# Kernel optimization log

Hardware: AMD Instinct MI355X
Metric: run time of the kernel (lower is better)

Reference implementation:

```python
import jax, jax.numpy as jnp
import numpy as np

N_HEAD = 16
LN_EPS = 1e-5


def _layernorm(x, g, b):
    mu = jnp.mean(x, axis=-1, keepdims=True)
    var = jnp.mean(jnp.square(x - mu), axis=-1, keepdims=True)
    return (x - mu) * jax.lax.rsqrt(var + LN_EPS) * g + b


def setup_inputs() -> dict:
    key = jax.random.key(0)
    ks = jax.random.split(key, 12)
    B, S, D = 2, 2048, 1024
    F = 4 * D
    std = 0.02
    return {
        "x": jax.random.normal(ks[0], (B, S, D), jnp.float32),
        "w_attn": jax.random.normal(ks[1], (D, 3 * D), jnp.float32) * std,
        "b_attn": jnp.zeros((3 * D,), jnp.float32),
        "w_o": jax.random.normal(ks[2], (D, D), jnp.float32) * std,
        "b_o": jnp.zeros((D,), jnp.float32),
        "ln1_g": jnp.ones((D,), jnp.float32),
        "ln1_b": jnp.zeros((D,), jnp.float32),
        "w_fc": jax.random.normal(ks[3], (D, F), jnp.float32) * std,
        "b_fc": jnp.zeros((F,), jnp.float32),
        "w_pr": jax.random.normal(ks[4], (F, D), jnp.float32) * std,
        "b_pr": jnp.zeros((D,), jnp.float32),
        "ln2_g": jnp.ones((D,), jnp.float32),
        "ln2_b": jnp.zeros((D,), jnp.float32),
    }


def reference(x, w_attn, b_attn, w_o, b_o, ln1_g, ln1_b,
              w_fc, b_fc, w_pr, b_pr, ln2_g, ln2_b):
    B, S, D = x.shape
    H = N_HEAD
    hd = D // H

    # --- attention ---
    qkv = x @ w_attn + b_attn                      # [B,S,3D]
    q, k, v = jnp.split(qkv, 3, axis=-1)
    q = q.reshape(B, S, H, hd).transpose(0, 2, 1, 3)  # [B,H,S,hd]
    k = k.reshape(B, S, H, hd).transpose(0, 2, 1, 3)
    v = v.reshape(B, S, H, hd).transpose(0, 2, 1, 3)

    # scores in fp32, scaled by sqrt(head_dim) (scale=True)
    w = jnp.einsum('bhqd,bhkd->bhqk', q.astype(jnp.float32),
                   k.astype(jnp.float32)) / jnp.sqrt(jnp.float32(hd))
    bias = jnp.tril(jnp.ones((S, S), jnp.float32))     # causal mask slice of registered buffer
    w = w * bias + (-10000.0) * (1.0 - bias)
    a = jax.nn.softmax(w, axis=-1).astype(v.dtype)
    o = jnp.einsum('bhqk,bhkd->bhqd', a, v)            # [B,H,S,hd]
    o = o.transpose(0, 2, 1, 3).reshape(B, S, D)
    a_out = o @ w_o + b_o

    # --- post-LN residual + MLP (gelu, d_ff = 4D) ---
    n = _layernorm(x + a_out, ln1_g, ln1_b)
    m = jax.nn.gelu(n @ w_fc + b_fc, approximate=False) @ w_pr + b_pr
    h = _layernorm(n + m, ln2_g, ln2_b)
    return h
```

## Files before the change

kernel.cpp:

```cpp
#include <hip/hip_runtime.h>
#include <stdint.h>
#include <math.h>


typedef __attribute__((ext_vector_type(4))) float f32x4;
typedef __attribute__((ext_vector_type(8))) short s16x8;

__device__ __forceinline__ float bf2f(short s){
  unsigned u = ((unsigned)(unsigned short)s) << 16;
  return __builtin_bit_cast(float, u);
}
__device__ __forceinline__ short f2bf(float f){
  unsigned u = __builtin_bit_cast(unsigned, f);
  unsigned r = (u + 0x7fffu + ((u >> 16) & 1u)) >> 16;
  return (short)(unsigned short)r;
}

__device__ __forceinline__ void gload_lds16(const void* gp, void* lp){
  __builtin_amdgcn_global_load_lds(
      (__attribute__((address_space(1))) void*)const_cast<void*>(gp),
      (__attribute__((address_space(3))) void*)lp,
      16, 0, 0);
}

__global__ void cvt_f32_bf16(const float* __restrict__ in, short* __restrict__ out, int n){
  int i = (blockIdx.x * blockDim.x + threadIdx.x) * 4;
  if (i < n){
    float4 v = *(const float4*)(in + i);
    short4 o;
    o.x = f2bf(v.x); o.y = f2bf(v.y); o.z = f2bf(v.z); o.w = f2bf(v.w);
    *(short4*)(out + i) = o;
  }
}

__global__ __launch_bounds__(256) void wtrans(const float* __restrict__ in,
                                              short* __restrict__ out, int R, int C){
  __shared__ float tile[32][33];
  int c0 = blockIdx.x * 32, r0 = blockIdx.y * 32;
  int tx = threadIdx.x, ty = threadIdx.y;
  #pragma unroll
  for (int j = 0; j < 4; ++j)
    tile[ty + j*8][tx] = in[(size_t)(r0 + ty + j*8) * C + c0 + tx];
  __syncthreads();
  #pragma unroll
  for (int j = 0; j < 4; ++j)
    out[(size_t)(c0 + ty + j*8) * R + r0 + tx] = f2bf(tile[tx][ty + j*8]);
}

__global__ __launch_bounds__(256) void vtrans(const short* __restrict__ qkv,
                                              short* __restrict__ vt){
  __shared__ short tile[32][33];
  int bh = blockIdx.z; int b = bh >> 4, h = bh & 15;
  int s0 = blockIdx.x * 32, d0 = blockIdx.y * 32;
  int tx = threadIdx.x, ty = threadIdx.y;
  #pragma unroll
  for (int j = 0; j < 4; ++j)
    tile[ty + j*8][tx] = qkv[(size_t)(b*2048 + s0 + ty + j*8) * 3072 + 2048 + h*64 + d0 + tx];
  __syncthreads();
  #pragma unroll
  for (int j = 0; j < 4; ++j)
    vt[(size_t)(bh*64 + d0 + ty + j*8) * 2048 + s0 + tx] = tile[tx][ty + j*8];
}

#define GBM 128
#define GBN 128
#define GBK 64

__global__ __launch_bounds__(256, 4) void gemm_bf16(
    const short* __restrict__ A, const short* __restrict__ BT,
    const float* __restrict__ bias,
    void* __restrict__ out, void* __restrict__ out2,
    void* __restrict__ out3, void* __restrict__ out4,
    int M, int N, int K, int EPI, int KS)
{
  __shared__ short sA[GBM * GBK];
  __shared__ short sB[GBN * GBK];
  const int t = threadIdx.x;
  const int lane = t & 63;
  const int w = t >> 6;
  const int wr = w >> 1, wc = w & 1;
  const int lrow = lane & 15;
  const int lk = lane >> 4;

  const int gx = gridDim.x;
  const int nwg = gx * gridDim.y;
  const int P = blockIdx.y * gx + blockIdx.x;
  const int wg = (P & 7) * (nwg >> 3) + (P >> 3);
  const int m0 = (wg / gx) * GBM, n0 = (wg % gx) * GBN;

  const int Kspl = K / KS;
  const int kbeg = blockIdx.z * Kspl;

  f32x4 acc[4][4] = {};

  for (int kk = kbeg; kk < kbeg + Kspl; kk += GBK){
    __syncthreads();
    #pragma unroll
    for (int r = 0; r < 4; ++r){
      int o = r * 4096 + t * 16;
      int row = o >> 7;
      int phys = (o >> 4) & 7;
      int lsl = phys ^ (row & 7);
      gload_lds16(A + (size_t)(m0 + row) * K + kk + lsl * 8, (char*)sA + o);
    }
    #pragma unroll
    for (int r = 0; r < 4; ++r){
      int o = r * 4096 + t * 16;
      int row = o >> 7;
      int phys = (o >> 4) & 7;
      int lsl = phys ^ (row & 7);
      gload_lds16(BT + (size_t)(n0 + row) * K + kk + lsl * 8, (char*)sB + o);
    }
    __syncthreads();

    #pragma unroll
    for (int kc = 0; kc < 2; ++kc){
      s16x8 af[4], bf[4];
      #pragma unroll
      for (int rt = 0; rt < 4; ++rt){
        int row = wr*64 + rt*16 + lrow;
        int slot = (kc*4 + lk) ^ (row & 7);
        af[rt] = *(const s16x8*)&sA[row*64 + slot*8];
      }
      #pragma unroll
      for (int ct = 0; ct < 4; ++ct){
        int row = wc*64 + ct*16 + lrow;
        int slot = (kc*4 + lk) ^ (row & 7);
        bf[ct] = *(const s16x8*)&sB[row*64 + slot*8];
      }
      #pragma unroll
      for (int rt = 0; rt < 4; ++rt)
        #pragma unroll
        for (int ct = 0; ct < 4; ++ct)
          acc[rt][ct] = __builtin_amdgcn_mfma_f32_16x16x32_bf16(af[rt], bf[ct], acc[rt][ct], 0, 0, 0);
    }
  }

  void* pz = (blockIdx.z == 0) ? out : (blockIdx.z == 1) ? out2
           : (blockIdx.z == 2) ? out3 : out4;
  #pragma unroll
  for (int rt = 0; rt < 4; ++rt){
    #pragma unroll
    for (int ct = 0; ct < 4; ++ct){
      #pragma unroll
      for (int r = 0; r < 4; ++r){
        int row = m0 + wr*64 + rt*16 + lk*4 + r;
        int col = n0 + wc*64 + ct*16 + lrow;
        size_t idx = (size_t)row * N + col;
        if (EPI == 4){
          ((short*)pz)[idx] = f2bf(acc[rt][ct][r]);
        } else {
          float v = acc[rt][ct][r] + bias[col];
          if (EPI == 0){
            ((short*)out)[idx] = f2bf(v);
          } else {
            float g = 0.5f * v * (1.0f + erff(v * 0.70710678118654752f));
            ((short*)out)[idx] = f2bf(g);
          }
        }
      }
    }
  }
}

__global__ __launch_bounds__(256, 2) void attn_kernel(
    const short* __restrict__ qkv, const short* __restrict__ vt,
    short* __restrict__ ob)
{
  const int P = blockIdx.x;
  const int xcd = P & 7;
  const int idx = P >> 3;
  const int raw = idx & 15;
  const int grp = idx >> 4;
  const int pairi = (grp & 2) ? (15 - raw) : raw;
  const int bh = xcd + (grp << 3);
  const int b = bh >> 4, h = bh & 15;
  const int t  = threadIdx.x;
  const int lane = t & 63;
  const int w = t >> 6;
  const int lrow = lane & 15, lk = lane >> 4;

  __shared__ short sK[2][64*64];
  __shared__ short sV[2][64*64];
  __shared__ short sP[4][16][68];

  const size_t kgbase = (size_t)(b*2048)*3072 + 1024 + h*64;
  const size_t vgbase = (size_t)((b*16 + h)*64)*2048;

  s16x8 bones;
  #pragma unroll
  for (int i = 0; i < 8; ++i) bones[i] = (short)0x3F80;

  auto stage = [&](int buf, int k0){
    #pragma unroll
    for (int r2 = 0; r2 < 2; ++r2){
      int o = r2*4096 + t*16;
      int row = o >> 7;
      int lsl = ((o >> 4) & 7) ^ (row & 7);
      gload_lds16(qkv + kgbase + (size_t)(k0 + row)*3072 + lsl*8, (char*)sK[buf] + o);
      gload_lds16(vt  + vgbase + (size_t)row*2048 + k0   + lsl*8, (char*)sV[buf] + o);
    }
  };

  const int qtA = pairi;
  const int qtB = 31 - pairi;
  const int qbaseA = qtA*64 + w*16;
  const int qbaseB = qtB*64 + w*16;

  s16x8 aqA[2], aqB[2];
  #pragma unroll
  for (int kc = 0; kc < 2; ++kc){
    aqA[kc] = *(const s16x8*)(qkv + (size_t)(b*2048 + qbaseA + lrow)*3072 + h*64 + kc*32 + lk*8);
    aqB[kc] = *(const s16x8*)(qkv + (size_t)(b*2048 + qbaseB + lrow)*3072 + h*64 + kc*32 + lk*8);
  }

  f32x4 oaccA[4] = {}, oaccB[4] = {};
  f32x4 sumA = {}, sumB = {};

  const int ntA = qtA + 1;
  const int ntB = qtB + 1;
  stage(0, 0);
  int cur = 0;

  for (int ktile = 0; ktile < ntB; ++ktile){
    const int k0 = ktile * 64;
    if (ktile + 1 < ntB){
      stage(cur ^ 1, k0 + 64);
      asm volatile("s_waitcnt vmcnt(4)" ::: "memory");
    } else {
      asm volatile("s_waitcnt vmcnt(0)" ::: "memory");
    }
    __builtin_amdgcn_s_barrier();
    __builtin_amdgcn_sched_barrier(0);

    {
      f32x4 sacc[4] = {};
      __builtin_amdgcn_s_setprio(1);
      #pragma unroll
      for (int kc = 0; kc < 2; ++kc){
        #pragma unroll
        for (int ct = 0; ct < 4; ++ct){
          int row = ct*16 + lrow;
          int slot = (kc*4 + lk) ^ (row & 7);
          s16x8 bk = *(const s16x8*)&sK[cur][row*64 + slot*8];
          sacc[ct] = __builtin_amdgcn_mfma_f32_16x16x32_bf16(aqB[kc], bk, sacc[ct], 0, 0, 0);
        }
      }
      __builtin_amdgcn_s_setprio(0);

      const bool need_mask = (k0 + 63 > qbaseB);
      #pragma unroll
      for (int ct = 0; ct < 4; ++ct){
        #pragma unroll
        for (int r = 0; r < 4; ++r){
          float v = sacc[ct][r] * 0.125f;
          if (need_mask){
            int qi = qbaseB + lk*4 + r;
            int ki = k0 + ct*16 + lrow;
            if (ki > qi) v = -10000.0f;
          }
          sP[w][lk*4 + r][ct*16 + lrow] = f2bf(__expf(v));
        }
      }

      s16x8 pa[2];
      #pragma unroll
      for (int kc = 0; kc < 2; ++kc)
        pa[kc] = *(const s16x8*)&sP[w][lrow][kc*32 + lk*8];
      __builtin_amdgcn_s_setprio(1);
      #pragma unroll
      for (int dt = 0; dt < 4; ++dt){
        #pragma unroll
        for (int kc = 0; kc < 2; ++kc){
          int row = dt*16 + lrow;
          int slot = (kc*4 + lk) ^ (row & 7);
          s16x8 bv = *(const s16x8*)&sV[cur][row*64 + slot*8];
          oaccB[dt] = __builtin_amdgcn_mfma_f32_16x16x32_bf16(pa[kc], bv, oaccB[dt], 0, 0, 0);
        }
      }
      #pragma unroll
      for (int kc = 0; kc < 2; ++kc)
        sumB = __builtin_amdgcn_mfma_f32_16x16x32_bf16(pa[kc], bones, sumB, 0, 0, 0);
      __builtin_amdgcn_s_setprio(0);
    }

    if (ktile < ntA){
      f32x4 sacc[4] = {};
      __builtin_amdgcn_s_setprio(1);
      #pragma unroll
      for (int kc = 0; kc < 2; ++kc){
        #pragma unroll
        for (int ct = 0; ct < 4; ++ct){
          int row = ct*16 + lrow;
          int slot = (kc*4 + lk) ^ (row & 7);
          s16x8 bk = *(const s16x8*)&sK[cur][row*64 + slot*8];
          sacc[ct] = __builtin_amdgcn_mfma_f32_16x16x32_bf16(aqA[kc], bk, sacc[ct], 0, 0, 0);
        }
      }
      __builtin_amdgcn_s_setprio(0);

      const bool need_mask = (k0 + 63 > qbaseA);
      #pragma unroll
      for (int ct = 0; ct < 4; ++ct){
        #pragma unroll
        for (int r = 0; r < 4; ++r){
          float v = sacc[ct][r] * 0.125f;
          if (need_mask){
            int qi = qbaseA + lk*4 + r;
            int ki = k0 + ct*16 + lrow;
            if (ki > qi) v = -10000.0f;
          }
          sP[w][lk*4 + r][ct*16 + lrow] = f2bf(__expf(v));
        }
      }

      s16x8 pa[2];
      #pragma unroll
      for (int kc = 0; kc < 2; ++kc)
        pa[kc] = *(const s16x8*)&sP[w][lrow][kc*32 + lk*8];
      __builtin_amdgcn_s_setprio(1);
      #pragma unroll
      for (int dt = 0; dt < 4; ++dt){
        #pragma unroll
        for (int kc = 0; kc < 2; ++kc){
          int row = dt*16 + lrow;
          int slot = (kc*4 + lk) ^ (row & 7);
          s16x8 bv = *(const s16x8*)&sV[cur][row*64 + slot*8];
          oaccA[dt] = __builtin_amdgcn_mfma_f32_16x16x32_bf16(pa[kc], bv, oaccA[dt], 0, 0, 0);
        }
      }
      #pragma unroll
      for (int kc = 0; kc < 2; ++kc)
        sumA = __builtin_amdgcn_mfma_f32_16x16x32_bf16(pa[kc], bones, sumA, 0, 0, 0);
      __builtin_amdgcn_s_setprio(0);
    }

    __builtin_amdgcn_sched_barrier(0);
    __builtin_amdgcn_s_barrier();
    cur ^= 1;
  }

  #pragma unroll
  for (int r = 0; r < 4; ++r){
    float invA = 1.0f / sumA[r];
    float invB = 1.0f / sumB[r];
    int rowA = b*2048 + qbaseA + lk*4 + r;
    int rowB = b*2048 + qbaseB + lk*4 + r;
    #pragma unroll
    for (int dt = 0; dt < 4; ++dt){
      int col = h*64 + dt*16 + lrow;
      ob[(size_t)rowA * 1024 + col] = f2bf(oaccA[dt][r] * invA);
      ob[(size_t)rowB * 1024 + col] = f2bf(oaccB[dt][r] * invB);
    }
  }
}

__global__ __launch_bounds__(256) void ln_fused(
    const short* __restrict__ p0, const short* __restrict__ p1,
    const short* __restrict__ p2, const short* __restrict__ p3,
    const float* __restrict__ bias,
    const short* __restrict__ resid_bf, const float* __restrict__ resid_f,
    const float* __restrict__ g, const float* __restrict__ b,
    void* __restrict__ out, int bf16_out)
{
  const int row = blockIdx.x;
  const int t = threadIdx.x;
  const size_t base = (size_t)row*1024 + t*4;
  short4 a0 = *(const short4*)(p0 + base);
  short4 a1 = *(const short4*)(p1 + base);
  short4 a2 = *(const short4*)(p2 + base);
  short4 a3 = *(const short4*)(p3 + base);
  float4 bi = *(const float4*)(bias + t*4);
  float r0, r1, r2, r3;
  if (resid_bf){
    short4 rr = *(const short4*)(resid_bf + base);
    r0 = bf2f(rr.x); r1 = bf2f(rr.y); r2 = bf2f(rr.z); r3 = bf2f(rr.w);
  } else {
    float4 rr = *(const float4*)(resid_f + base);
    r0 = rr.x; r1 = rr.y; r2 = rr.z; r3 = rr.w;
  }
  float v0 = bf2f(a0.x) + bf2f(a1.x) + bf2f(a2.x) + bf2f(a3.x) + bi.x + r0;
  float v1 = bf2f(a0.y) + bf2f(a1.y) + bf2f(a2.y) + bf2f(a3.y) + bi.y + r1;
  float v2 = bf2f(a0.z) + bf2f(a1.z) + bf2f(a2.z) + bf2f(a3.z) + bi.z + r2;
  float v3 = bf2f(a0.w) + bf2f(a1.w) + bf2f(a2.w) + bf2f(a3.w) + bi.w + r3;
  float s = v0 + v1 + v2 + v3;
  float q = v0*v0 + v1*v1 + v2*v2 + v3*v3;
  #pragma unroll
  for (int off = 1; off < 64; off <<= 1){
    s += __shfl_xor(s, off, 64);
    q += __shfl_xor(q, off, 64);
  }
  __shared__ float ss[4], sq[4];
  if ((t & 63) == 0){ ss[t >> 6] = s; sq[t >> 6] = q; }
  __syncthreads();
  s = ss[0] + ss[1] + ss[2] + ss[3];
  q = sq[0] + sq[1] + sq[2] + sq[3];
  float mu = s * (1.0f/1024.0f);
  float var = q * (1.0f/1024.0f) - mu*mu;
  float rs = rsqrtf(var + 1e-5f);
  float4 gg = *(const float4*)(g + t*4);
  float4 bb = *(const float4*)(b + t*4);
  float o0 = (v0 - mu)*rs*gg.x + bb.x;
  float o1 = (v1 - mu)*rs*gg.y + bb.y;
  float o2 = (v2 - mu)*rs*gg.z + bb.z;
  float o3 = (v3 - mu)*rs*gg.w + bb.w;
  if (bf16_out){
    short4 o; o.x = f2bf(o0); o.y = f2bf(o1); o.z = f2bf(o2); o.w = f2bf(o3);
    *(short4*)((short*)out + base) = o;
  } else {
    float4 o = {o0, o1, o2, o3};
    *(float4*)((float*)out + base) = o;
  }
}

extern "C" void kernel_launch(void* const* d_in, const int* in_sizes, int n_in,
                              void* d_out, int out_size, void* d_ws, size_t ws_size,
                              hipStream_t stream) {
  const float* x      = (const float*)d_in[0];
  const float* w_attn = (const float*)d_in[1];
  const float* b_attn = (const float*)d_in[2];
  const float* w_o    = (const float*)d_in[3];
  const float* b_o    = (const float*)d_in[4];
  const float* ln1_g  = (const float*)d_in[5];
  const float* ln1_b  = (const float*)d_in[6];
  const float* w_fc   = (const float*)d_in[7];
  const float* b_fc   = (const float*)d_in[8];
  const float* w_pr   = (const float*)d_in[9];
  const float* b_pr   = (const float*)d_in[10];
  const float* ln2_g  = (const float*)d_in[11];
  const float* ln2_b  = (const float*)d_in[12];

  char* ws = (char*)d_ws;
  const size_t MB = 1048576;
  short* waT  = (short*)(ws + 0);
  short* wfT  = (short*)(ws + 6*MB);
  short* wpT  = (short*)(ws + 14*MB);
  short* woT  = (short*)(ws + 22*MB);
  short* xb   = (short*)(ws + 24*MB);
  short* vt   = (short*)(ws + 24*MB);
  short* pp2  = (short*)(ws + 24*MB);
  short* qkvb = (short*)(ws + 32*MB);
  short* fb   = (short*)(ws + 32*MB);
  short* ob   = (short*)(ws + 56*MB);
  short* pp0  = (short*)(ws + 64*MB);
  short* pp1  = (short*)(ws + 72*MB);
  short* nb   = (short*)(ws + 80*MB);
  short* pp3  = (short*)(ws + 88*MB);

  const int M = 4096;

  cvt_f32_bf16<<<dim3(M*1024/1024), dim3(256), 0, stream>>>(x, xb, M*1024);
  wtrans<<<dim3(3072/32, 1024/32), dim3(32,8), 0, stream>>>(w_attn, waT, 1024, 3072);
  wtrans<<<dim3(1024/32, 1024/32), dim3(32,8), 0, stream>>>(w_o,   woT, 1024, 1024);
  wtrans<<<dim3(4096/32, 1024/32), dim3(32,8), 0, stream>>>(w_fc,  wfT, 1024, 4096);
  wtrans<<<dim3(1024/32, 4096/32), dim3(32,8), 0, stream>>>(w_pr,  wpT, 4096, 1024);
  gemm_bf16<<<dim3(3072/GBN, M/GBM), dim3(256), 0, stream>>>(
      xb, waT, b_attn, qkvb, nullptr, nullptr, nullptr, M, 3072, 1024, 0, 1);
  vtrans<<<dim3(2048/32, 64/32, 32), dim3(32,8), 0, stream>>>(qkvb, vt);
  attn_kernel<<<dim3(512), dim3(256), 0, stream>>>(qkvb, vt, ob);
  gemm_bf16<<<dim3(1024/GBN, M/GBM, 4), dim3(256), 0, stream>>>(
      ob, woT, nullptr, pp0, pp1, pp2, pp3, M, 1024, 1024, 4, 4);
  ln_fused<<<dim3(M), dim3(256), 0, stream>>>(pp0, pp1, pp2, pp3, b_o,
                                              nullptr, x, ln1_g, ln1_b, nb, 1);
  gemm_bf16<<<dim3(4096/GBN, M/GBM), dim3(256), 0, stream>>>(
      nb, wfT, b_fc, fb, nullptr, nullptr, nullptr, M, 4096, 1024, 2, 1);
  gemm_bf16<<<dim3(1024/GBN, M/GBM, 4), dim3(256), 0, stream>>>(
      fb, wpT, nullptr, pp0, pp1, pp2, pp3, M, 1024, 4096, 4, 4);
  ln_fused<<<dim3(M), dim3(256), 0, stream>>>(pp0, pp1, pp2, pp3, b_pr,
                                              nb, nullptr, ln2_g, ln2_b, d_out, 0);
}
```

Measured before the change: 255.1 us.

## Stage GEMM epilogue through LDS for vector stores and prefold softmax scale into Q

The GEMM epilogue now writes the bf16 results into a swizzled LDS buffer that reuses the A/B tiles, then copies them to global memory with coalesced 16-byte stores in place of scattered 2-byte stores. In the QKV GEMM epilogue the Q columns are multiplied by 0.125*log2(e), so the attention kernel can drop its per-element scale and use exp2f. The mask value changes to keep masked entries near zero in base 2. This adds two barriers and LDS traffic per tile, and the store path assumes full tiles with no bounds checks.

Result: no change. 255.8 us (+0.3%).

```diff
diff --git a/kernel.cpp b/kernel.cpp
--- a/kernel.cpp
+++ b/kernel.cpp
@@ -22,6 +22,8 @@
       (__attribute__((address_space(3))) void*)lp,
       16, 0, 0);
 }
+
+#define QSCALE 0.18033688f
 
 __global__ void cvt_f32_bf16(const float* __restrict__ in, short* __restrict__ out, int n){
   int i = (blockIdx.x * blockDim.x + threadIdx.x) * 4;
@@ -73,8 +75,9 @@
     void* __restrict__ out3, void* __restrict__ out4,
     int M, int N, int K, int EPI, int KS)
 {
-  __shared__ short sA[GBM * GBK];
-  __shared__ short sB[GBN * GBK];
+  __shared__ __attribute__((aligned(16))) short smem[GBM*GBK*2];
+  short* sA = smem;
+  short* sB = smem + GBM*GBK;
   const int t = threadIdx.x;
   const int lane = t & 63;
   const int w = t >> 6;
@@ -136,30 +139,41 @@
     }
   }
 
+  __syncthreads();
+  #pragma unroll
+  for (int rt = 0; rt < 4; ++rt){
+    #pragma unroll
+    for (int ct = 0; ct < 4; ++ct){
+      #pragma unroll
+      for (int r = 0; r < 4; ++r){
+        int row = wr*64 + rt*16 + lk*4 + r;
+        int col = wc*64 + ct*16 + lrow;
+        float v = acc[rt][ct][r];
+        if (EPI != 4){
+          v += bias[n0 + col];
+          if (EPI == 0){
+            if (n0 + col < 1024) v *= QSCALE;
+          } else {
+            v = 0.5f * v * (1.0f + erff(v * 0.70710678118654752f));
+          }
+        }
+        int off = row*256 + ((col*2) ^ (((row >> 2) & 7) << 5));
+        *(short*)((char*)smem + off) = f2bf(v);
+      }
+    }
+  }
+  __syncthreads();
   void* pz = (blockIdx.z == 0) ? out : (blockIdx.z == 1) ? out2
            : (blockIdx.z == 2) ? out3 : out4;
-  #pragma unroll
-  for (int rt = 0; rt < 4; ++rt){
-    #pragma unroll
-    for (int ct = 0; ct < 4; ++ct){
-      #pragma unroll
-      for (int r = 0; r < 4; ++r){
-        int row = m0 + wr*64 + rt*16 + lk*4 + r;
-        int col = n0 + wc*64 + ct*16 + lrow;
-        size_t idx = (size_t)row * N + col;
-        if (EPI == 4){
-          ((short*)pz)[idx] = f2bf(acc[rt][ct][r]);
-        } else {
-          float v = acc[rt][ct][r] + bias[col];
-          if (EPI == 0){
-            ((short*)out)[idx] = f2bf(v);
-          } else {
-            float g = 0.5f * v * (1.0f + erff(v * 0.70710678118654752f));
-            ((short*)out)[idx] = f2bf(g);
-          }
-        }
-      }
-    }
+  short* outp = (short*)pz;
+  #pragma unroll
+  for (int j = 0; j < 8; ++j){
+    int L = j*4096 + t*16;
+    int row = L >> 8;
+    int cb  = L & 255;
+    int phys = row*256 + (cb ^ (((row >> 2) & 7) << 5));
+    s16x8 vv = *(const s16x8*)((char*)smem + phys);
+    *(s16x8*)(outp + (size_t)(m0 + row) * N + n0 + (cb >> 1)) = vv;
   }
 }
 
@@ -253,13 +267,13 @@
       for (int ct = 0; ct < 4; ++ct){
         #pragma unroll
         for (int r = 0; r < 4; ++r){
-          float v = sacc[ct][r] * 0.125f;
+          float v = sacc[ct][r];
           if (need_mask){
             int qi = qbaseB + lk*4 + r;
             int ki = k0 + ct*16 + lrow;
-            if (ki > qi) v = -10000.0f;
+            if (ki > qi) v = -100000.0f;
           }
-          sP[w][lk*4 + r][ct*16 + lrow] = f2bf(__expf(v));
+          sP[w][lk*4 + r][ct*16 + lrow] = f2bf(exp2f(v));
         }
       }
 
@@ -304,13 +318,13 @@
       for (int ct = 0; ct < 4; ++ct){
         #pragma unroll
         for (int r = 0; r < 4; ++r){
-          float v = sacc[ct][r] * 0.125f;
+          float v = sacc[ct][r];
           if (need_mask){
             int qi = qbaseA + lk*4 + r;
             int ki = k0 + ct*16 + lrow;
-            if (ki > qi) v = -10000.0f;
+            if (ki > qi) v = -100000.0f;
           }
-          sP[w][lk*4 + r][ct*16 + lrow] = f2bf(__expf(v));
+          sP[w][lk*4 + r][ct*16 + lrow] = f2bf(exp2f(v));
         }
       }
 
```
